# Kernel optimization log

Measured on AMD Instinct MI355X. Metric: run time of the kernel, lower is better.

Reference implementation:

```python
import jax, jax.numpy as jnp
import numpy as np
from jax import lax

B, IN, HID, OUT = 32, 1024, 1024, 1024
NN, NS, NH = 1000, 64, 4          # n_paths/num_neurons, num_states, attn heads
NSTEPS = NS * 10                   # 640 SDE steps
GROUPS = 10                        # python loop groups in original BICEPLayer
T_HORIZON = 1.0


def setup_inputs() -> dict:
    key = jax.random.key(0)
    ks = jax.random.split(key, 16)
    def n(k, shape, s=0.02):
        return jax.random.normal(k, shape, jnp.float32) * s
    z = lambda *s: jnp.zeros(s, jnp.float32)
    return {
        "x": jax.random.normal(ks[0], (B, IN), jnp.float32),
        "noise": jax.random.normal(ks[1], (B, NN, NSTEPS), jnp.float32),
        "W_emb": n(ks[2], (NN * NS, IN)), "b_emb": z(NN * NS),
        "w_ih": n(ks[3], (4 * NS, NS), 0.1), "w_hh": n(ks[4], (4 * NS, NS), 0.1),
        "b_ih": z(4 * NS), "b_hh": z(4 * NS),
        "w_in": n(ks[5], (3 * NS, NS), 0.1), "b_in": z(3 * NS),
        "w_out": n(ks[6], (NS, NS), 0.1), "b_out": z(NS),
        "W_fix": jax.random.normal(ks[7], (HID, NS), jnp.float32),  # torch.randn dim-fix linear
        "W_inproj": n(ks[8], (NN, IN)), "b_inproj": z(NN),
        "conv_w": n(ks[9], (1, NSTEPS + 1, 3), 0.05), "conv_b": z(1),
        "W_bout": n(ks[10], (HID, NN)), "b_bout": z(HID),
        "decay_rate": jnp.float32(0.1),
        "W_fuse": n(ks[11], (HID, 2 * HID)), "b_fuse": z(HID),
        "W_proj": n(ks[12], (OUT, HID)), "b_proj": z(OUT),
    }


def _forward(x, noise, W_emb, b_emb, w_ih, w_hh, b_ih, b_hh, w_in, b_in,
             w_out, b_out, W_fix, W_inproj, b_inproj, conv_w, conv_b,
             W_bout, b_bout, decay_rate, W_fuse, b_fuse, W_proj, b_proj):
    Bsz = x.shape[0]
    # ---- ENN branch ----
    ns = (x @ W_emb.T + b_emb).reshape(Bsz, NN, NS)

    def lstm_step(carry, xt):  # xt [B, NS]
        h, c = carry
        g = xt @ w_ih.T + b_ih + h @ w_hh.T + b_hh
        i, f, gg, o = jnp.split(g, 4, axis=-1)  # torch gate order i,f,g,o
        c = jax.nn.sigmoid(f) * c + jax.nn.sigmoid(i) * jnp.tanh(gg)
        h = jax.nn.sigmoid(o) * jnp.tanh(c)
        return (h, c), h

    h0 = jnp.zeros((Bsz, NS), x.dtype)
    _, hs = lax.scan(lstm_step, (h0, h0), jnp.swapaxes(ns, 0, 1))
    lstm_out = jnp.swapaxes(hs, 0, 1)  # [B, NN, NS]

    qkv = lstm_out @ w_in.T + b_in
    q, k, v = jnp.split(qkv, 3, axis=-1)
    dh = NS // NH
    heads = lambda t: t.reshape(Bsz, NN, NH, dh).transpose(0, 2, 1, 3)
    q, k, v = heads(q), heads(k), heads(v)
    scores = jnp.einsum('bhqd,bhkd->bhqk', q, k) * (1.0 / float(np.sqrt(dh)))
    attn = jax.nn.softmax(scores, axis=-1)
    ctx = jnp.einsum('bhqk,bhkd->bhqd', attn, v).transpose(0, 2, 1, 3).reshape(Bsz, NN, NS)
    attended = ctx @ w_out.T + b_out
    attn_w = attn.mean(axis=1)  # torch MHA averages heads by default

    enn = jax.nn.relu(attended.mean(axis=1))  # [B, NS]
    enn = enn @ W_fix.T                        # [B, HID] (random dim-fix linear, no bias)

    # ---- BICEP branch (vectorized Brownian SDE over all batches/paths) ----
    fb = jax.nn.sigmoid(x @ W_inproj.T + b_inproj)  # [B, NN]
    # original uses .item() -> detached scalars, only first 10 feedback values
    f_full = jnp.repeat(lax.stop_gradient(fb[:, :GROUPS]), NN // GROUPS, axis=1)  # [B, NN]
    dt = T_HORIZON / NSTEPS
    sq = float(np.sqrt(dt))
    dr = lax.stop_gradient(decay_rate)  # .item() in original

    def sde_step(Xc, nt):  # Euler-Maruyama: dX = -decay*X dt + feedback dW
        Xn = Xc * (1.0 - dr * dt) + f_full * sq * nt
        return Xn, Xn

    _, Xs = lax.scan(sde_step, jnp.zeros((Bsz, NN), x.dtype), jnp.moveaxis(noise, 2, 0))
    paths = jnp.concatenate([jnp.zeros((1, Bsz, NN), x.dtype), Xs], axis=0)  # [T+1, B, NN]
    paths = jnp.moveaxis(paths, 0, 1)  # [B, NSTEPS+1, NN] -> channels = time

    agg = lax.conv_general_dilated(paths, conv_w, (1,), ((1, 1),),
                                   dimension_numbers=('NCH', 'OIH', 'NCH'))
    agg = agg[:, 0, :] + conv_b  # [B, NN]
    bicep = agg @ W_bout.T + b_bout  # [B, HID]

    # ---- fusion (dropout is identity in eval) ----
    fused = jnp.concatenate([enn, bicep], axis=-1) @ W_fuse.T + b_fuse
    output = fused @ W_proj.T + b_proj
    return output, enn, bicep, attn_w


def reference(x, noise, W_emb, b_emb, w_ih, w_hh, b_ih, b_hh, w_in, b_in,
              w_out, b_out, W_fix, W_inproj, b_inproj, conv_w, conv_b,
              W_bout, b_bout, decay_rate, W_fuse, b_fuse, W_proj, b_proj):
    return _forward(x, noise, W_emb, b_emb, w_ih, w_hh, b_ih, b_hh, w_in, b_in,
                    w_out, b_out, W_fix, W_inproj, b_inproj, conv_w, conv_b,
                    W_bout, b_bout, decay_rate, W_fuse, b_fuse, W_proj, b_proj)
```

## Files before the change

### kernel.cpp

```cpp
#include <hip/hip_runtime.h>
#include <hip/hip_bf16.h>
#include <math.h>

#define BATCH 32
#define NNEUR 1000
#define NSTATE 64
#define INDIM 1024
#define HID 1024

typedef short bf16x8 __attribute__((ext_vector_type(8)));
typedef float f32x4 __attribute__((ext_vector_type(4)));

__device__ __forceinline__ float sigmoidf_(float x){ return 1.0f/(1.0f + __expf(-x)); }
__device__ __forceinline__ unsigned short f2bf(float x){
  unsigned u = __float_as_uint(x);
  unsigned r = (u + 0x7FFFu + ((u>>16)&1u)) >> 16;
  return (unsigned short)r;
}
__device__ __forceinline__ float sig2(float x){
  return __builtin_amdgcn_rcpf(1.0f + __builtin_amdgcn_exp2f(x * -1.44269504f));
}
__device__ __forceinline__ float tanh2(float x){
  return 1.0f - 2.0f*__builtin_amdgcn_rcpf(1.0f + __builtin_amdgcn_exp2f(x * 2.88539008f));
}
__device__ __forceinline__ f32x4 unpk4(uint2 p){
  f32x4 r;
  r[0] = __uint_as_float(p.x << 16);
  r[1] = __uint_as_float(p.x & 0xffff0000u);
  r[2] = __uint_as_float(p.y << 16);
  r[3] = __uint_as_float(p.y & 0xffff0000u);
  return r;
}

__global__ __launch_bounds__(256) void k1_emb(const float* __restrict__ x,
    const float* __restrict__ W_emb, const float* __restrict__ b_emb,
    const float* __restrict__ W_inp, const float* __restrict__ b_inp,
    float* __restrict__ ns, float* __restrict__ fb)
{
  __shared__ __align__(16) float xl[BATCH][256];
  __shared__ float red[32][33];
  const int tid = threadIdx.x;
  const int jt = tid >> 4;
  const int seg = tid & 15;
  const int j0 = blockIdx.x * 32;
  const float* wr_[2];
  #pragma unroll
  for (int jj=0;jj<2;jj++){
    int j = j0 + jt*2 + jj;
    if (j < 64000) wr_[jj] = W_emb + (size_t)j * INDIM;
    else { int t2 = j - 64000; if (t2 > 999) t2 = 999; wr_[jj] = W_inp + (size_t)t2 * INDIM; }
  }
  float acc[2][32];
  #pragma unroll
  for (int jj=0;jj<2;jj++)
    #pragma unroll
    for (int b=0;b<32;b++) acc[jj][b]=0.f;
  for (int c=0;c<4;c++){
    __syncthreads();
    for (int f = tid; f < 2048; f += 256){
      int b = f >> 6; int col = (f & 63) << 2;
      *(float4*)&xl[b][col] = *(const float4*)&x[b*INDIM + c*256 + col];
    }
    __syncthreads();
    #pragma unroll
    for (int ii=0; ii<4; ii++){
      float4 wv[2];
      #pragma unroll
      for (int jj=0;jj<2;jj++) wv[jj] = *(const float4*)&wr_[jj][c*256 + ii*64 + seg*4];
      #pragma unroll
      for (int b=0;b<32;b++){
        float4 xv = *(const float4*)&xl[b][ii*64 + seg*4];
        #pragma unroll
        for (int jj=0;jj<2;jj++){
          acc[jj][b] = fmaf(wv[jj].x, xv.x, acc[jj][b]);
          acc[jj][b] = fmaf(wv[jj].y, xv.y, acc[jj][b]);
          acc[jj][b] = fmaf(wv[jj].z, xv.z, acc[jj][b]);
          acc[jj][b] = fmaf(wv[jj].w, xv.w, acc[jj][b]);
        }
      }
    }
  }
  #pragma unroll
  for (int jj=0;jj<2;jj++){
    #pragma unroll
    for (int b=0;b<32;b++){
      float v = acc[jj][b];
      v += __shfl_xor(v, 1);
      v += __shfl_xor(v, 2);
      v += __shfl_xor(v, 4);
      v += __shfl_xor(v, 8);
      if (seg == 0) red[jt*2+jj][b] = v;
    }
  }
  __syncthreads();
  #pragma unroll
  for (int it=0; it<4; it++){
    int idx = it*256 + tid;
    int b = idx >> 5, jl = idx & 31;
    int jg = j0 + jl;
    float v = red[jl][b];
    if (jg < 64000){
      ns[(size_t)b*64000 + jg] = v + b_emb[jg];
    } else if (jg < 65000){
      fb[b*1000 + (jg-64000)] = sigmoidf_(v + b_inp[jg-64000]);
    }
  }
}

__global__ __launch_bounds__(256) void k2_pre(const float* __restrict__ ns,
   const float* __restrict__ w_ih, const float* __restrict__ b_ih, const float* __restrict__ b_hh,
   unsigned short* __restrict__ preh)
{
  __shared__ __align__(16) float nsl[64*64];
  const int tid = threadIdx.x;
  const int j = tid;
  const int rn0 = blockIdx.x * 64;
  const int pcol = (j & 63)*4 + (j >> 6);
  float wreg[64];
  const float* wr = w_ih + j*64;
  #pragma unroll
  for (int k=0;k<64;k+=4){
    float4 v = *(const float4*)&wr[k];
    wreg[k]=v.x; wreg[k+1]=v.y; wreg[k+2]=v.z; wreg[k+3]=v.w;
  }
  float bias = b_ih[j] + b_hh[j];
  const float4* src = (const float4*)(ns + (size_t)rn0*64);
  for (int i=tid; i<64*16; i+=256) ((float4*)nsl)[i] = src[i];
  __syncthreads();
  for (int r=0;r<64;r++){
    float a0=0,a1=0,a2=0,a3=0;
    #pragma unroll
    for (int k=0;k<64;k+=4){
      float4 nv = *(const float4*)&nsl[r*64+k];
      a0=fmaf(nv.x,wreg[k],a0);   a1=fmaf(nv.y,wreg[k+1],a1);
      a2=fmaf(nv.z,wreg[k+2],a2); a3=fmaf(nv.w,wreg[k+3],a3);
    }
    preh[(size_t)(rn0+r)*256 + pcol] = f2bf((a0+a1)+(a2+a3) + bias);
  }
}

__global__ __launch_bounds__(256) void k3_lstm_sde(
  const unsigned short* __restrict__ preh, unsigned short* __restrict__ lstmT,
  const float* __restrict__ w_hh,
  const float* __restrict__ noise, const float* __restrict__ fb,
  const float* __restrict__ conv_w, const float* __restrict__ decay_p,
  float* __restrict__ S0, float* __restrict__ S1, float* __restrict__ S2)
{
  __shared__ __align__(16) unsigned char shraw[8192];
  const int tid = threadIdx.x;
  if (blockIdx.x < 8){
    unsigned short* hls = (unsigned short*)shraw;
    const int b0 = blockIdx.x * 4;
    const int w = tid >> 6;
    const int lane = tid & 63;
    const int nl = lane & 15;
    const int g  = lane >> 4;
    const int r  = nl & 3;
    for (int i = tid; i < 640; i += 256) hls[i] = 0;
    bf16x8 A[4][2];
    #pragma unroll
    for (int tt=0; tt<4; tt++){
      const int rt = 4*w + tt;
      const float* wsrc = w_hh + (size_t)((nl&3)*64 + 4*rt + (nl>>2))*64;
      #pragma unroll
      for (int kh=0; kh<2; kh++){
        bf16x8 f;
        #pragma unroll
        for (int i=0;i<8;i++) f[i] = (short)f2bf(wsrc[kh*32 + 8*g + i]);
        A[tt][kh] = f;
      }
    }
    const int jg = 16*w + 4*(nl>>2) + g;
    const int bat = b0 + r;
    const unsigned short* pp = preh + (size_t)bat*256000 + jg*4;
    uint2 P[4];
    #pragma unroll
    for (int s=0;s<4;s++) P[s] = *(const uint2*)(pp + (size_t)s*256);
    const int rdA = r*80 + (g ^ r)*8;
    const int wr = r*80 + ((jg>>3) ^ r)*8 + (jg & 7);
    unsigned short* lt = lstmT + ((size_t)bat*64 + jg)*1000;
    const bool s1 = (nl & 4) != 0, s2 = (nl & 8) != 0;
    float c = 0.f;
    unsigned ph[4];
    __syncthreads();
    int buf = 0;
    for (int tb=0; tb<1000; tb+=8){
      #pragma unroll
      for (int u=0;u<8;u++){
        bf16x8 B0 = *(const bf16x8*)&hls[buf*320 + rdA];
        bf16x8 B1 = *(const bf16x8*)&hls[buf*320 + rdA + 32];
        const int slot = u & 3;
        f32x4 Cp = unpk4(P[slot]);
        int tp = tb + u + 4; if (tp > 999) tp = 999;
        P[slot] = *(const uint2*)(pp + (size_t)tp*256);
        f32x4 D0 = __builtin_amdgcn_mfma_f32_16x16x32_bf16(A[0][0], B0, Cp, 0,0,0);
        D0 = __builtin_amdgcn_mfma_f32_16x16x32_bf16(A[0][1], B1, D0, 0,0,0);
        f32x4 D1 = __builtin_amdgcn_mfma_f32_16x16x32_bf16(A[1][0], B0, Cp, 0,0,0);
        D1 = __builtin_amdgcn_mfma_f32_16x16x32_bf16(A[1][1], B1, D1, 0,0,0);
        f32x4 D2 = __builtin_amdgcn_mfma_f32_16x16x32_bf16(A[2][0], B0, Cp, 0,0,0);
        D2 = __builtin_amdgcn_mfma_f32_16x16x32_bf16(A[2][1], B1, D2, 0,0,0);
        f32x4 D3 = __builtin_amdgcn_mfma_f32_16x16x32_bf16(A[3][0], B0, Cp, 0,0,0);
        D3 = __builtin_amdgcn_mfma_f32_16x16x32_bf16(A[3][1], B1, D3, 0,0,0);
        float g0 = s2 ? (s1 ? D3[0] : D2[0]) : (s1 ? D1[0] : D0[0]);
        float g1 = s2 ? (s1 ? D3[1] : D2[1]) : (s1 ? D1[1] : D0[1]);
        float g2 = s2 ? (s1 ? D3[2] : D2[2]) : (s1 ? D1[2] : D0[2]);
        float g3 = s2 ? (s1 ? D3[3] : D2[3]) : (s1 ? D1[3] : D0[3]);
        float iv = sig2(g0), fv = sig2(g1), gv = tanh2(g2), ov = sig2(g3);
        c = fv*c + iv*gv;
        float h = ov * tanh2(c);
        unsigned hb = f2bf(h);
        if (u & 1) ph[u>>1] |= hb << 16; else ph[u>>1] = hb;
        hls[(buf^1)*320 + wr] = (unsigned short)hb;
        asm volatile("s_waitcnt lgkmcnt(0)" ::: "memory");
        __builtin_amdgcn_s_barrier();
        asm volatile("" ::: "memory");
        buf ^= 1;
      }
      *(uint4*)(lt + tb) = make_uint4(ph[0], ph[1], ph[2], ph[3]);
    }
  } else {
    float* cw = (float*)shraw;
    for (int f = tid; f < 641*3; f += 256) cw[f] = conv_w[f];
    __syncthreads();
    int idx = (blockIdx.x - 8)*256 + tid;
    if (idx < 32000){
      int b = idx / 1000, n = idx - b*1000;
      float fcoef = fb[b*1000 + (n/100)];
      float dr = decay_p[0];
      const float dt = 1.0f/640.0f;
      float adec = 1.0f - dr*dt;
      float g = fcoef * sqrtf(dt);
      const float* nptr = noise + (size_t)idx * 640;
      float X=0.f, s0=0.f, s1=0.f, s2=0.f;
      for (int t0=0;t0<640;t0+=4){
        float4 nz = *(const float4*)&nptr[t0];
        float nv[4] = {nz.x, nz.y, nz.z, nz.w};
        #pragma unroll
        for (int u=0;u<4;u++){
          X = fmaf(adec, X, g*nv[u]);
          int t = t0 + u + 1;
          s0 = fmaf(cw[t*3+0], X, s0);
          s1 = fmaf(cw[t*3+1], X, s1);
          s2 = fmaf(cw[t*3+2], X, s2);
        }
      }
      S0[idx]=s0; S1[idx]=s1; S2[idx]=s2;
    }
  }
}

__global__ __launch_bounds__(256) void k4_qkv(const unsigned short* __restrict__ lstmT,
  const float* __restrict__ w_in, const float* __restrict__ b_in,
  unsigned short* __restrict__ Qb, unsigned short* __restrict__ Kb, unsigned short* __restrict__ Vt)
{
  __shared__ __align__(16) float wl[192*64];
  __shared__ float bl[192];
  const int tid = threadIdx.x;
  for (int i=tid;i<3072;i+=256) ((float4*)wl)[i] = ((const float4*)w_in)[i];
  if (tid < 192) bl[tid] = b_in[tid];
  __syncthreads();
  const int rl = tid & 127, dh = tid >> 7;
  const int rn = blockIdx.x*128 + rl;
  const int b = rn >> 10, n = rn & 1023;
  const bool valid = (n < 1000);
  const int nc = valid ? n : 999;
  float row[64];
  #pragma unroll
  for (int k=0;k<64;k++){
    unsigned v = lstmT[((size_t)b*64 + k)*1000 + nc];
    row[k] = valid ? __uint_as_float(v << 16) : 0.f;
  }
  for (int dc=0; dc<12; dc++){
    const int d0 = dh*96 + dc*8;
    float acc[8];
    #pragma unroll
    for (int u=0;u<8;u++) acc[u] = bl[d0+u];
    #pragma unroll
    for (int k=0;k<64;k+=4){
      float4 rv = *(const float4*)&row[k];
      #pragma unroll
      for (int u=0;u<8;u++){
        float4 wv = *(const float4*)&wl[(d0+u)*64 + k];
        acc[u]=fmaf(rv.x,wv.x,acc[u]); acc[u]=fmaf(rv.y,wv.y,acc[u]);
        acc[u]=fmaf(rv.z,wv.z,acc[u]); acc[u]=fmaf(rv.w,wv.w,acc[u]);
      }
    }
    unsigned short pk[8];
    #pragma unroll
    for (int u=0;u<8;u++) pk[u] = valid ? f2bf(acc[u]) : (unsigned short)0;
    if (d0 + 8 <= 64){
      *(bf16x8*)&Qb[(size_t)rn*64 + d0] = *(bf16x8*)pk;
    } else if (d0 + 8 <= 128){
      *(bf16x8*)&Kb[(size_t)rn*64 + (d0-64)] = *(bf16x8*)pk;
    } else {
      int dv = d0 - 128;
      #pragma unroll
      for (int u=0;u<8;u++) Vt[((size_t)b*64 + dv+u)*1024 + n] = pk[u];
    }
  }
}

__global__ __launch_bounds__(256) void k5_attn(
  const unsigned short* __restrict__ Qb, const unsigned short* __restrict__ Kb,
  const unsigned short* __restrict__ Vt,
  float* __restrict__ attn_w, float* __restrict__ ctx)
{
  const int b = blockIdx.x;
  const int qblk = blockIdx.y;
  const int wid = threadIdx.x >> 6;
  const int lane = threadIdx.x & 63;
  const int r = lane & 15, gq = lane >> 4;
  const int q = qblk*64 + wid*16 + r;
  const bool gok = (gq < 2);
  const float SC2 = 0.25f * 1.44269504f;
  const f32x4 z4 = {0.f,0.f,0.f,0.f};

  bf16x8 qf[4];
  #pragma unroll
  for (int h=0; h<4; h++){
    bf16x8 f = {};
    if (gok) f = *(const bf16x8*)&Qb[(((size_t)b*1024)+q)*64 + h*16 + 8*gq];
    qf[h] = f;
  }
  float snv[4];
  #pragma unroll
  for (int h=0; h<4; h++){
    float es = 0.f;
    for (int kk=0; kk<63; kk++){
      bf16x8 kf = {};
      if (gok) kf = *(const bf16x8*)&Kb[(((size_t)b*1024)+(kk*16+r))*64 + h*16 + 8*gq];
      f32x4 d = __builtin_amdgcn_mfma_f32_16x16x32_bf16(kf, qf[h], z4, 0,0,0);
      float e0=__builtin_amdgcn_exp2f(d[0]*SC2), e1=__builtin_amdgcn_exp2f(d[1]*SC2);
      float e2=__builtin_amdgcn_exp2f(d[2]*SC2), e3=__builtin_amdgcn_exp2f(d[3]*SC2);
      if (kk == 62 && !gok){ e0=0;e1=0;e2=0;e3=0; }
      es += (e0+e1)+(e2+e3);
    }
    es += __shfl_xor(es, 16);
    es += __shfl_xor(es, 32);
    snv[h] = 0.25f / es;
  }
  f32x4 cacc[4] = {};
  float* awrow = attn_w + (size_t)b*1000000;
  for (int kkp=0; kkp<31; kkp++){
    const int kk = kkp*2;
    f32x4 aacc0 = z4, aacc1 = z4;
    #pragma unroll
    for (int h=0; h<4; h++){
      bf16x8 kf0 = {}, kf1 = {};
      if (gok){
        kf0 = *(const bf16x8*)&Kb[(((size_t)b*1024)+(kk*16+r))*64 + h*16 + 8*gq];
        kf1 = *(const bf16x8*)&Kb[(((size_t)b*1024)+(kk*16+16+r))*64 + h*16 + 8*gq];
      }
      f32x4 d0 = __builtin_amdgcn_mfma_f32_16x16x32_bf16(kf0, qf[h], z4, 0,0,0);
      f32x4 d1 = __builtin_amdgcn_mfma_f32_16x16x32_bf16(kf1, qf[h], z4, 0,0,0);
      float p00=__builtin_amdgcn_exp2f(d0[0]*SC2)*snv[h], p01=__builtin_amdgcn_exp2f(d0[1]*SC2)*snv[h];
      float p02=__builtin_amdgcn_exp2f(d0[2]*SC2)*snv[h], p03=__builtin_amdgcn_exp2f(d0[3]*SC2)*snv[h];
      float p10=__builtin_amdgcn_exp2f(d1[0]*SC2)*snv[h], p11=__builtin_amdgcn_exp2f(d1[1]*SC2)*snv[h];
      float p12=__builtin_amdgcn_exp2f(d1[2]*SC2)*snv[h], p13=__builtin_amdgcn_exp2f(d1[3]*SC2)*snv[h];
      aacc0[0]+=p00; aacc0[1]+=p01; aacc0[2]+=p02; aacc0[3]+=p03;
      aacc1[0]+=p10; aacc1[1]+=p11; aacc1[2]+=p12; aacc1[3]+=p13;
      const int slo = (r + 32*gq) & 63;
      const int shi = (slo + 16) & 63;
      {
        unsigned pa = (unsigned)f2bf(p00) | ((unsigned)f2bf(p01) << 16);
        unsigned pb = (unsigned)f2bf(p02) | ((unsigned)f2bf(p03) << 16);
        int b0_ = __shfl((int)pa, slo), b1_ = __shfl((int)pb, slo);
        int b2_ = __shfl((int)pa, shi), b3_ = __shfl((int)pb, shi);
        union { int i[4]; bf16x8 v; } pu;
        pu.i[0]=b0_; pu.i[1]=b1_; pu.i[2]=b2_; pu.i[3]=b3_;
        bf16x8 pfrag = pu.v;
        if (!gok) pfrag = (bf16x8){};
        bf16x8 vf = {};
        if (gok) vf = *(const bf16x8*)&Vt[(((size_t)b*64) + h*16 + r)*1024 + kk*16 + 8*gq];
        cacc[h] = __builtin_amdgcn_mfma_f32_16x16x32_bf16(vf, pfrag, cacc[h], 0,0,0);
      }
      {
        unsigned pa = (unsigned)f2bf(p10) | ((unsigned)f2bf(p11) << 16);
        unsigned pb = (unsigned)f2bf(p12) | ((unsigned)f2bf(p13) << 16);
        int b0_ = __shfl((int)pa, slo), b1_ = __shfl((int)pb, slo);
        int b2_ = __shfl((int)pa, shi), b3_ = __shfl((int)pb, shi);
        union { int i[4]; bf16x8 v; } pu;
        pu.i[0]=b0_; pu.i[1]=b1_; pu.i[2]=b2_; pu.i[3]=b3_;
        bf16x8 pfrag = pu.v;
        if (!gok) pfrag = (bf16x8){};
        bf16x8 vf = {};
        if (gok) vf = *(const bf16x8*)&Vt[(((size_t)b*64) + h*16 + r)*1024 + kk*16 + 16 + 8*gq];
        cacc[h] = __builtin_amdgcn_mfma_f32_16x16x32_bf16(vf, pfrag, cacc[h], 0,0,0);
      }
    }
    if (q < 1000){
      *(f32x4*)&awrow[(size_t)q*1000 + kk*16 + 4*gq] = aacc0;
      *(f32x4*)&awrow[(size_t)q*1000 + kk*16 + 16 + 4*gq] = aacc1;
    }
  }
  {
    const int kk = 62;
    f32x4 aacc = z4;
    #pragma unroll
    for (int h=0; h<4; h++){
      bf16x8 kf = {};
      if (gok) kf = *(const bf16x8*)&Kb[(((size_t)b*1024)+(kk*16+r))*64 + h*16 + 8*gq];
      f32x4 d = __builtin_amdgcn_mfma_f32_16x16x32_bf16(kf, qf[h], z4, 0,0,0);
      float p0=__builtin_amdgcn_exp2f(d[0]*SC2)*snv[h], p1=__builtin_amdgcn_exp2f(d[1]*SC2)*snv[h];
      float p2=__builtin_amdgcn_exp2f(d[2]*SC2)*snv[h], p3=__builtin_amdgcn_exp2f(d[3]*SC2)*snv[h];
      if (!gok){ p0=0;p1=0;p2=0;p3=0; }
      aacc[0]+=p0; aacc[1]+=p1; aacc[2]+=p2; aacc[3]+=p3;
      unsigned pa = (unsigned)f2bf(p0) | ((unsigned)f2bf(p1) << 16);
      unsigned pb = (unsigned)f2bf(p2) | ((unsigned)f2bf(p3) << 16);
      int slo = (r + 32*gq) & 63;
      int shi = (slo + 16) & 63;
      int b0_ = __shfl((int)pa, slo), b1_ = __shfl((int)pb, slo);
      int b2_ = __shfl((int)pa, shi), b3_ = __shfl((int)pb, shi);
      union { int i[4]; bf16x8 v; } pu;
      pu.i[0]=b0_; pu.i[1]=b1_; pu.i[2]=b2_; pu.i[3]=b3_;
      bf16x8 pfrag = pu.v;
      if (!gok) pfrag = (bf16x8){};
      bf16x8 vf = {};
      if (gok) vf = *(const bf16x8*)&Vt[(((size_t)b*64) + h*16 + r)*1024 + kk*16 + 8*gq];
      cacc[h] = __builtin_amdgcn_mfma_f32_16x16x32_bf16(vf, pfrag, cacc[h], 0,0,0);
    }
    if (q < 1000 && gok){
      *(f32x4*)&awrow[(size_t)q*1000 + kk*16 + 4*gq] = aacc;
    }
  }
  if (q < 1000){
    #pragma unroll
    for (int h=0; h<4; h++){
      f32x4 cv = cacc[h];
      cv[0]*=4.f; cv[1]*=4.f; cv[2]*=4.f; cv[3]*=4.f;
      *(f32x4*)&ctx[(((size_t)b*1024)+q)*64 + h*16 + 4*gq] = cv;
    }
  }
}

__global__ __launch_bounds__(256) void k6a_psum(const float* __restrict__ ctx,
  float* __restrict__ psum)
{
  __shared__ float part[256];
  const int blk = blockIdx.x;
  const int b = blk >> 3, seg = blk & 7;
  const int t = threadIdx.x, d = t & 63, sg = t >> 6;
  float s = 0.f;
  const int nend = seg*125 + 125;
  for (int n = seg*125 + sg; n < nend; n += 4)
    s += ctx[(((size_t)b*1024)+n)*64 + d];
  part[t] = s;
  __syncthreads();
  if (t < 64) psum[((size_t)b*8 + seg)*64 + t] = part[t] + part[64+t] + part[128+t] + part[192+t];
}

__global__ __launch_bounds__(256) void k6b_enn(const float* __restrict__ psum,
  const float* __restrict__ w_out, const float* __restrict__ b_out,
  const float* __restrict__ W_fix, float* __restrict__ enn_out)
{
  __shared__ __align__(16) float csum[64];
  __shared__ __align__(16) float epre[64];
  int b = blockIdx.x, t = threadIdx.x;
  if (t < 64){
    float a = 0;
    #pragma unroll
    for (int s2=0;s2<8;s2++) a += psum[((size_t)b*8 + s2)*64 + t];
    csum[t] = a;
  }
  __syncthreads();
  if (t < 64){
    const float* wr = w_out + t*64;
    float a = 0;
    #pragma unroll
    for (int k=0;k<64;k++) a = fmaf(csum[k], wr[k], a);
    epre[t] = fmaxf(a*(1.0f/1000.0f) + b_out[t], 0.0f);
  }
  __syncthreads();
  for (int m = t; m < 1024; m += 256){
    const float* fr = W_fix + m*64;
    float a = 0;
    #pragma unroll
    for (int k=0;k<64;k+=4){
      float4 e4 = *(const float4*)&epre[k];
      float4 f4 = *(const float4*)&fr[k];
      a=fmaf(e4.x,f4.x,a); a=fmaf(e4.y,f4.y,a); a=fmaf(e4.z,f4.z,a); a=fmaf(e4.w,f4.w,a);
    }
    enn_out[b*1024 + m] = a;
  }
}

__global__ __launch_bounds__(256) void k7_agg(const float* __restrict__ S0, const float* __restrict__ S1,
  const float* __restrict__ S2, const float* __restrict__ conv_b, float* __restrict__ agg)
{
  int i = blockIdx.x*256 + threadIdx.x;
  if (i >= 32000) return;
  int n = i % 1000;
  float v = S1[i] + conv_b[0];
  if (n > 0)   v += S0[i-1];
  if (n < 999) v += S2[i+1];
  agg[i] = v;
}

__global__ __launch_bounds__(256) void k8_bicep(const float* __restrict__ agg,
  const float* __restrict__ W_bout, const float* __restrict__ b_bout, float* __restrict__ bicep)
{
  int gt = blockIdx.x*256 + threadIdx.x;
  int bb = gt & 31, m = gt >> 5;
  const float* wr = W_bout + (size_t)m*1000;
  const float* ar = agg + bb*1000;
  float a = 0;
  for (int n=0;n<1000;n+=4){
    float4 w4 = *(const float4*)&wr[n];
    float4 a4 = *(const float4*)&ar[n];
    a=fmaf(w4.x,a4.x,a); a=fmaf(w4.y,a4.y,a); a=fmaf(w4.z,a4.z,a); a=fmaf(w4.w,a4.w,a);
  }
  bicep[bb*1024 + m] = a + b_bout[m];
}

__global__ __launch_bounds__(256) void k9_fuse(const float* __restrict__ enn, const float* __restrict__ bic,
  const float* __restrict__ W_fuse, const float* __restrict__ b_fuse, float* __restrict__ fused)
{
  int gt = blockIdx.x*256 + threadIdx.x;
  int bb = gt & 31, m = gt >> 5;
  const float* er = enn + bb*1024;
  const float* br = bic + bb*1024;
  const float* wr = W_fuse + (size_t)m*2048;
  float a = 0;
  for (int jj=0;jj<1024;jj+=4){
    float4 e4 = *(const float4*)&er[jj];
    float4 w4 = *(const float4*)&wr[jj];
    a=fmaf(e4.x,w4.x,a); a=fmaf(e4.y,w4.y,a); a=fmaf(e4.z,w4.z,a); a=fmaf(e4.w,w4.w,a);
  }
  for (int jj=0;jj<1024;jj+=4){
    float4 b4 = *(const float4*)&br[jj];
    float4 w4 = *(const float4*)&wr[1024+jj];
    a=fmaf(b4.x,w4.x,a); a=fmaf(b4.y,w4.y,a); a=fmaf(b4.z,w4.z,a); a=fmaf(b4.w,w4.w,a);
  }
  fused[bb*1024 + m] = a + b_fuse[m];
}

__global__ __launch_bounds__(256) void k10_proj(const float* __restrict__ fused,
  const float* __restrict__ W_proj, const float* __restrict__ b_proj, float* __restrict__ outp)
{
  int gt = blockIdx.x*256 + threadIdx.x;
  int bb = gt & 31, m = gt >> 5;
  const float* fr = fused + bb*1024;
  const float* wr = W_proj + (size_t)m*1024;
  float a = 0;
  for (int jj=0;jj<1024;jj+=4){
    float4 f4 = *(const float4*)&fr[jj];
    float4 w4 = *(const float4*)&wr[jj];
    a=fmaf(f4.x,w4.x,a); a=fmaf(f4.y,w4.y,a); a=fmaf(f4.z,w4.z,a); a=fmaf(f4.w,w4.w,a);
  }
  outp[bb*1024 + m] = a + b_proj[m];
}

extern "C" void kernel_launch(void* const* d_in, const int* in_sizes, int n_in,
                              void* d_out, int out_size, void* d_ws, size_t ws_size,
                              hipStream_t stream)
{
  const float* x       = (const float*)d_in[0];
  const float* noise   = (const float*)d_in[1];
  const float* W_emb   = (const float*)d_in[2];
  const float* b_emb   = (const float*)d_in[3];
  const float* w_ih    = (const float*)d_in[4];
  const float* w_hh    = (const float*)d_in[5];
  const float* b_ih    = (const float*)d_in[6];
  const float* b_hh    = (const float*)d_in[7];
  const float* w_in    = (const float*)d_in[8];
  const float* b_in    = (const float*)d_in[9];
  const float* w_out   = (const float*)d_in[10];
  const float* b_out   = (const float*)d_in[11];
  const float* W_fix   = (const float*)d_in[12];
  const float* W_inp   = (const float*)d_in[13];
  const float* b_inp   = (const float*)d_in[14];
  const float* conv_w  = (const float*)d_in[15];
  const float* conv_b  = (const float*)d_in[16];
  const float* W_bout  = (const float*)d_in[17];
  const float* b_bout  = (const float*)d_in[18];
  const float* decay   = (const float*)d_in[19];
  const float* W_fuse  = (const float*)d_in[20];
  const float* b_fuse  = (const float*)d_in[21];
  const float* W_proj  = (const float*)d_in[22];
  const float* b_proj  = (const float*)d_in[23];

  float* out       = (float*)d_out;
  float* enn_out   = out + 32768;
  float* bicep_out = out + 65536;
  float* attn_out  = out + 98304;

  float* ws    = (float*)d_ws;
  float* fb    = ws;
  float* ns    = ws + 32000;
  unsigned short* preh  = (unsigned short*)(ws + 2080000);
  float* psum  = ws + 6200000;
  unsigned short* lstmT = (unsigned short*)(ws + 10272000);
  float* ctx   = ws + 12320000;
  float* S0    = ws + 14417152;
  float* S1    = ws + 14449152;
  float* S2    = ws + 14481152;
  float* agg   = ws + 14513152;
  float* fused = ws + 14545152;
  unsigned short* Qb = (unsigned short*)(ws + 14577920);
  unsigned short* Kb = Qb + 2097152;
  unsigned short* Vt = Kb + 2097152;

  k1_emb<<<2032, 256, 0, stream>>>(x, W_emb, b_emb, W_inp, b_inp, ns, fb);
  k2_pre<<<500, 256, 0, stream>>>(ns, w_ih, b_ih, b_hh, preh);
  k3_lstm_sde<<<133, 256, 0, stream>>>(preh, lstmT, w_hh, noise, fb, conv_w, decay, S0, S1, S2);
  k4_qkv<<<256, 256, 0, stream>>>(lstmT, w_in, b_in, Qb, Kb, Vt);
  k5_attn<<<dim3(32,16), 256, 0, stream>>>(Qb, Kb, Vt, attn_out, ctx);
  k6a_psum<<<256, 256, 0, stream>>>(ctx, psum);
  k6b_enn<<<32, 256, 0, stream>>>(psum, w_out, b_out, W_fix, enn_out);
  k7_agg<<<126, 256, 0, stream>>>(S0, S1, S2, conv_b, agg);
  k8_bicep<<<128, 256, 0, stream>>>(agg, W_bout, b_bout, bicep_out);
  k9_fuse<<<128, 256, 0, stream>>>(enn_out, bicep_out, W_fuse, b_fuse, fused);
  k10_proj<<<128, 256, 0, stream>>>(fused, W_proj, b_proj, out);
}
```

Before: 972.0 us.

## Fuse embedding GEMM with LSTM input projection and merge independent tail kernels

```diff
diff --git a/kernel.cpp b/kernel.cpp
--- a/kernel.cpp
+++ b/kernel.cpp
@@ -3,10 +3,6 @@
 #include <math.h>
 
 #define BATCH 32
-#define NNEUR 1000
-#define NSTATE 64
-#define INDIM 1024
-#define HID 1024
 
 typedef short bf16x8 __attribute__((ext_vector_type(8)));
 typedef float f32x4 __attribute__((ext_vector_type(4)));
@@ -32,46 +28,48 @@
   return r;
 }
 
-__global__ __launch_bounds__(256) void k1_emb(const float* __restrict__ x,
+__global__ __launch_bounds__(256) void k12_emb_pre(const float* __restrict__ x,
     const float* __restrict__ W_emb, const float* __restrict__ b_emb,
     const float* __restrict__ W_inp, const float* __restrict__ b_inp,
-    float* __restrict__ ns, float* __restrict__ fb)
+    const float* __restrict__ w_ih, const float* __restrict__ b_ih, const float* __restrict__ b_hh,
+    float* __restrict__ fb, unsigned short* __restrict__ preh)
 {
   __shared__ __align__(16) float xl[BATCH][256];
-  __shared__ float red[32][33];
+  __shared__ float red[64][33];
+  __shared__ __align__(16) float nsl2[32][68];
   const int tid = threadIdx.x;
   const int jt = tid >> 4;
   const int seg = tid & 15;
-  const int j0 = blockIdx.x * 32;
-  const float* wr_[2];
-  #pragma unroll
-  for (int jj=0;jj<2;jj++){
-    int j = j0 + jt*2 + jj;
-    if (j < 64000) wr_[jj] = W_emb + (size_t)j * INDIM;
-    else { int t2 = j - 64000; if (t2 > 999) t2 = 999; wr_[jj] = W_inp + (size_t)t2 * INDIM; }
-  }
-  float acc[2][32];
-  #pragma unroll
-  for (int jj=0;jj<2;jj++)
+  const int blk = blockIdx.x;
+  const bool isemb = (blk < 1000);
+  const float* wr_[4];
+  #pragma unroll
+  for (int jj=0;jj<4;jj++){
+    if (isemb) wr_[jj] = W_emb + (size_t)(blk*64 + jt*4 + jj) * 1024;
+    else { int t2 = (blk-1000)*64 + jt*4 + jj; if (t2 > 999) t2 = 999; wr_[jj] = W_inp + (size_t)t2 * 1024; }
+  }
+  float acc[4][32];
+  #pragma unroll
+  for (int jj=0;jj<4;jj++)
     #pragma unroll
     for (int b=0;b<32;b++) acc[jj][b]=0.f;
   for (int c=0;c<4;c++){
     __syncthreads();
     for (int f = tid; f < 2048; f += 256){
       int b = f >> 6; int col = (f & 63) << 2;
-      *(float4*)&xl[b][col] = *(const float4*)&x[b*INDIM + c*256 + col];
+      *(float4*)&xl[b][col] = *(const float4*)&x[b*1024 + c*256 + col];
     }
     __syncthreads();
     #pragma unroll
     for (int ii=0; ii<4; ii++){
-      float4 wv[2];
-      #pragma unroll
-      for (int jj=0;jj<2;jj++) wv[jj] = *(const float4*)&wr_[jj][c*256 + ii*64 + seg*4];
+      float4 wv[4];
+      #pragma unroll
+      for (int jj=0;jj<4;jj++) wv[jj] = *(const float4*)&wr_[jj][c*256 + ii*64 + seg*4];
       #pragma unroll
       for (int b=0;b<32;b++){
         float4 xv = *(const float4*)&xl[b][ii*64 + seg*4];
         #pragma unroll
-        for (int jj=0;jj<2;jj++){
+        for (int jj=0;jj<4;jj++){
           acc[jj][b] = fmaf(wv[jj].x, xv.x, acc[jj][b]);
           acc[jj][b] = fmaf(wv[jj].y, xv.y, acc[jj][b]);
           acc[jj][b] = fmaf(wv[jj].z, xv.z, acc[jj][b]);
@@ -81,7 +79,7 @@
     }
   }
   #pragma unroll
-  for (int jj=0;jj<2;jj++){
+  for (int jj=0;jj<4;jj++){
     #pragma unroll
     for (int b=0;b<32;b++){
       float v = acc[jj][b];
@@ -89,32 +87,25 @@
       v += __shfl_xor(v, 2);
       v += __shfl_xor(v, 4);
       v += __shfl_xor(v, 8);
-      if (seg == 0) red[jt*2+jj][b] = v;
+      if (seg == 0) red[jt*4+jj][b] = v;
     }
   }
   __syncthreads();
   #pragma unroll
-  for (int it=0; it<4; it++){
+  for (int it=0; it<8; it++){
     int idx = it*256 + tid;
-    int b = idx >> 5, jl = idx & 31;
-    int jg = j0 + jl;
+    int b = idx >> 6, jl = idx & 63;
     float v = red[jl][b];
-    if (jg < 64000){
-      ns[(size_t)b*64000 + jg] = v + b_emb[jg];
-    } else if (jg < 65000){
-      fb[b*1000 + (jg-64000)] = sigmoidf_(v + b_inp[jg-64000]);
-    }
-  }
-}
-
-__global__ __launch_bounds__(256) void k2_pre(const float* __restrict__ ns,
-   const float* __restrict__ w_ih, const float* __restrict__ b_ih, const float* __restrict__ b_hh,
-   unsigned short* __restrict__ preh)
-{
-  __shared__ __align__(16) float nsl[64*64];
-  const int tid = threadIdx.x;
+    if (isemb){
+      nsl2[b][jl] = v + b_emb[blk*64 + jl];
+    } else {
+      int jin = (blk-1000)*64 + jl;
+      if (jin < 1000) fb[b*1000 + jin] = sigmoidf_(v + b_inp[jin]);
+    }
+  }
+  if (!isemb) return;
+  __syncthreads();
   const int j = tid;
-  const int rn0 = blockIdx.x * 64;
   const int pcol = (j & 63)*4 + (j >> 6);
   float wreg[64];
   const float* wr = w_ih + j*64;
@@ -124,18 +115,15 @@
     wreg[k]=v.x; wreg[k+1]=v.y; wreg[k+2]=v.z; wreg[k+3]=v.w;
   }
   float bias = b_ih[j] + b_hh[j];
-  const float4* src = (const float4*)(ns + (size_t)rn0*64);
-  for (int i=tid; i<64*16; i+=256) ((float4*)nsl)[i] = src[i];
-  __syncthreads();
-  for (int r=0;r<64;r++){
+  for (int b=0;b<32;b++){
     float a0=0,a1=0,a2=0,a3=0;
     #pragma unroll
     for (int k=0;k<64;k+=4){
-      float4 nv = *(const float4*)&nsl[r*64+k];
+      float4 nv = *(const float4*)&nsl2[b][k];
       a0=fmaf(nv.x,wreg[k],a0);   a1=fmaf(nv.y,wreg[k+1],a1);
       a2=fmaf(nv.z,wreg[k+2],a2); a3=fmaf(nv.w,wreg[k+3],a3);
     }
-    preh[(size_t)(rn0+r)*256 + pcol] = f2bf((a0+a1)+(a2+a3) + bias);
+    preh[(size_t)(b*1000+blk)*256 + pcol] = f2bf((a0+a1)+(a2+a3) + bias);
   }
 }
 
@@ -433,83 +421,83 @@
   }
 }
 
-__global__ __launch_bounds__(256) void k6a_psum(const float* __restrict__ ctx,
-  float* __restrict__ psum)
-{
-  __shared__ float part[256];
-  const int blk = blockIdx.x;
-  const int b = blk >> 3, seg = blk & 7;
-  const int t = threadIdx.x, d = t & 63, sg = t >> 6;
-  float s = 0.f;
-  const int nend = seg*125 + 125;
-  for (int n = seg*125 + sg; n < nend; n += 4)
-    s += ctx[(((size_t)b*1024)+n)*64 + d];
-  part[t] = s;
-  __syncthreads();
-  if (t < 64) psum[((size_t)b*8 + seg)*64 + t] = part[t] + part[64+t] + part[128+t] + part[192+t];
-}
-
-__global__ __launch_bounds__(256) void k6b_enn(const float* __restrict__ psum,
+__global__ __launch_bounds__(256) void k67_psum_agg(const float* __restrict__ ctx,
+  float* __restrict__ psum,
+  const float* __restrict__ S0, const float* __restrict__ S1,
+  const float* __restrict__ S2, const float* __restrict__ conv_b, float* __restrict__ agg)
+{
+  if (blockIdx.x < 256){
+    __shared__ float part[256];
+    const int blk = blockIdx.x;
+    const int b = blk >> 3, seg = blk & 7;
+    const int t = threadIdx.x, d = t & 63, sg = t >> 6;
+    float s = 0.f;
+    const int nend = seg*125 + 125;
+    for (int n = seg*125 + sg; n < nend; n += 4)
+      s += ctx[(((size_t)b*1024)+n)*64 + d];
+    part[t] = s;
+    __syncthreads();
+    if (t < 64) psum[((size_t)b*8 + seg)*64 + t] = part[t] + part[64+t] + part[128+t] + part[192+t];
+  } else {
+    int i = (blockIdx.x - 256)*256 + threadIdx.x;
+    if (i >= 32000) return;
+    int n = i % 1000;
+    float v = S1[i] + conv_b[0];
+    if (n > 0)   v += S0[i-1];
+    if (n < 999) v += S2[i+1];
+    agg[i] = v;
+  }
+}
+
+__global__ __launch_bounds__(256) void k68_enn_bicep(const float* __restrict__ psum,
   const float* __restrict__ w_out, const float* __restrict__ b_out,
-  const float* __restrict__ W_fix, float* __restrict__ enn_out)
-{
-  __shared__ __align__(16) float csum[64];
-  __shared__ __align__(16) float epre[64];
-  int b = blockIdx.x, t = threadIdx.x;
-  if (t < 64){
+  const float* __restrict__ W_fix, float* __restrict__ enn_out,
+  const float* __restrict__ agg, const float* __restrict__ W_bout,
+  const float* __restrict__ b_bout, float* __restrict__ bicep)
+{
+  if (blockIdx.x < 32){
+    __shared__ __align__(16) float csum[64];
+    __shared__ __align__(16) float epre[64];
+    int b = blockIdx.x, t = threadIdx.x;
+    if (t < 64){
+      float a = 0;
+      #pragma unroll
+      for (int s2=0;s2<8;s2++) a += psum[((size_t)b*8 + s2)*64 + t];
+      csum[t] = a;
+    }
+    __syncthreads();
+    if (t < 64){
+      const float* wr = w_out + t*64;
+      float a = 0;
+      #pragma unroll
+      for (int k=0;k<64;k++) a = fmaf(csum[k], wr[k], a);
+      epre[t] = fmaxf(a*(1.0f/1000.0f) + b_out[t], 0.0f);
+    }
+    __syncthreads();
+    for (int m = t; m < 1024; m += 256){
+      const float* fr = W_fix + m*64;
+      float a = 0;
+      #pragma unroll
+      for (int k=0;k<64;k+=4){
+        float4 e4 = *(const float4*)&epre[k];
+        float4 f4 = *(const float4*)&fr[k];
+        a=fmaf(e4.x,f4.x,a); a=fmaf(e4.y,f4.y,a); a=fmaf(e4.z,f4.z,a); a=fmaf(e4.w,f4.w,a);
+      }
+      enn_out[b*1024 + m] = a;
+    }
+  } else {
+    int gt = (blockIdx.x - 32)*256 + threadIdx.x;
+    int bb = gt & 31, m = gt >> 5;
+    const float* wr = W_bout + (size_t)m*1000;
+    const float* ar = agg + bb*1000;
     float a = 0;
-    #pragma unroll
-    for (int s2=0;s2<8;s2++) a += psum[((size_t)b*8 + s2)*64 + t];
-    csum[t] = a;
-  }
-  __syncthreads();
-  if (t < 64){
-    const float* wr = w_out + t*64;
-    float a = 0;
-    #pragma unroll
-    for (int k=0;k<64;k++) a = fmaf(csum[k], wr[k], a);
-    epre[t] = fmaxf(a*(1.0f/1000.0f) + b_out[t], 0.0f);
-  }
-  __syncthreads();
-  for (int m = t; m < 1024; m += 256){
-    const float* fr = W_fix + m*64;
-    float a = 0;
-    #pragma unroll
-    for (int k=0;k<64;k+=4){
-      float4 e4 = *(const float4*)&epre[k];
-      float4 f4 = *(const float4*)&fr[k];
-      a=fmaf(e4.x,f4.x,a); a=fmaf(e4.y,f4.y,a); a=fmaf(e4.z,f4.z,a); a=fmaf(e4.w,f4.w,a);
-    }
-    enn_out[b*1024 + m] = a;
-  }
-}
-
-__global__ __launch_bounds__(256) void k7_agg(const float* __restrict__ S0, const float* __restrict__ S1,
-  const float* __restrict__ S2, const float* __restrict__ conv_b, float* __restrict__ agg)
-{
-  int i = blockIdx.x*256 + threadIdx.x;
-  if (i >= 32000) return;
-  int n = i % 1000;
-  float v = S1[i] + conv_b[0];
-  if (n > 0)   v += S0[i-1];
-  if (n < 999) v += S2[i+1];
-  agg[i] = v;
-}
-
-__global__ __launch_bounds__(256) void k8_bicep(const float* __restrict__ agg,
-  const float* __restrict__ W_bout, const float* __restrict__ b_bout, float* __restrict__ bicep)
-{
-  int gt = blockIdx.x*256 + threadIdx.x;
-  int bb = gt & 31, m = gt >> 5;
-  const float* wr = W_bout + (size_t)m*1000;
-  const float* ar = agg + bb*1000;
-  float a = 0;
-  for (int n=0;n<1000;n+=4){
-    float4 w4 = *(const float4*)&wr[n];
-    float4 a4 = *(const float4*)&ar[n];
-    a=fmaf(w4.x,a4.x,a); a=fmaf(w4.y,a4.y,a); a=fmaf(w4.z,a4.z,a); a=fmaf(w4.w,a4.w,a);
-  }
-  bicep[bb*1024 + m] = a + b_bout[m];
+    for (int n=0;n<1000;n+=4){
+      float4 w4 = *(const float4*)&wr[n];
+      float4 a4 = *(const float4*)&ar[n];
+      a=fmaf(w4.x,a4.x,a); a=fmaf(w4.y,a4.y,a); a=fmaf(w4.z,a4.z,a); a=fmaf(w4.w,a4.w,a);
+    }
+    bicep[bb*1024 + m] = a + b_bout[m];
+  }
 }
 
 __global__ __launch_bounds__(256) void k9_fuse(const float* __restrict__ enn, const float* __restrict__ bic,
@@ -586,7 +574,6 @@
 
   float* ws    = (float*)d_ws;
   float* fb    = ws;
-  float* ns    = ws + 32000;
   unsigned short* preh  = (unsigned short*)(ws + 2080000);
   float* psum  = ws + 6200000;
   unsigned short* lstmT = (unsigned short*)(ws + 10272000);
@@ -600,15 +587,14 @@
   unsigned short* Kb = Qb + 2097152;
   unsigned short* Vt = Kb + 2097152;
 
-  k1_emb<<<2032, 256, 0, stream>>>(x, W_emb, b_emb, W_inp, b_inp, ns, fb);
-  k2_pre<<<500, 256, 0, stream>>>(ns, w_ih, b_ih, b_hh, preh);
+  k12_emb_pre<<<1016, 256, 0, stream>>>(x, W_emb, b_emb, W_inp, b_inp,
+                                        w_ih, b_ih, b_hh, fb, preh);
   k3_lstm_sde<<<133, 256, 0, stream>>>(preh, lstmT, w_hh, noise, fb, conv_w, decay, S0, S1, S2);
   k4_qkv<<<256, 256, 0, stream>>>(lstmT, w_in, b_in, Qb, Kb, Vt);
   k5_attn<<<dim3(32,16), 256, 0, stream>>>(Qb, Kb, Vt, attn_out, ctx);
-  k6a_psum<<<256, 256, 0, stream>>>(ctx, psum);
-  k6b_enn<<<32, 256, 0, stream>>>(psum, w_out, b_out, W_fix, enn_out);
-  k7_agg<<<126, 256, 0, stream>>>(S0, S1, S2, conv_b, agg);
-  k8_bicep<<<128, 256, 0, stream>>>(agg, W_bout, b_bout, bicep_out);
+  k67_psum_agg<<<382, 256, 0, stream>>>(ctx, psum, S0, S1, S2, conv_b, agg);
+  k68_enn_bicep<<<160, 256, 0, stream>>>(psum, w_out, b_out, W_fix, enn_out,
+                                         agg, W_bout, b_bout, bicep_out);
   k9_fuse<<<128, 256, 0, stream>>>(enn_out, bicep_out, W_fuse, b_fuse, fused);
   k10_proj<<<128, 256, 0, stream>>>(fused, W_proj, b_proj, out);
 }
```

After: 985.9 us. Within noise of the previous version (+1.4%).
